# Kernel optimization log

Hardware: AMD Instinct MI355X
Metric: run time of the kernel (lower is better)

Reference implementation:

```python
import jax, jax.numpy as jnp
import numpy as np


def euler_xyz_to_matrix(angles):
    # pytorch3d euler_angles_to_matrix(angles, 'XYZ') = R_X(a0) @ R_Y(a1) @ R_Z(a2)
    ax, ay, az = angles[..., 0], angles[..., 1], angles[..., 2]
    cx, sx = jnp.cos(ax), jnp.sin(ax)
    cy, sy = jnp.cos(ay), jnp.sin(ay)
    cz, sz = jnp.cos(az), jnp.sin(az)
    one = jnp.ones_like(ax)
    zero = jnp.zeros_like(ax)
    Rx = jnp.stack([one, zero, zero, zero, cx, -sx, zero, sx, cx], axis=-1).reshape(*ax.shape, 3, 3)
    Ry = jnp.stack([cy, zero, sy, zero, one, zero, -sy, zero, cy], axis=-1).reshape(*ax.shape, 3, 3)
    Rz = jnp.stack([cz, -sz, zero, sz, cz, zero, zero, zero, one], axis=-1).reshape(*ax.shape, 3, 3)
    return Rx @ Ry @ Rz


def chamfer_bidir(x, y):
    # x, y: [R, I, N, 3]. Squared-distance chamfer, mean point reduction, per (R,I) batch.
    x2 = jnp.sum(x * x, axis=-1)  # [R,I,N]
    y2 = jnp.sum(y * y, axis=-1)  # [R,I,N]
    # d2[r,i,n,m] = |x_n - y_m|^2
    d2 = x2[..., :, None] + y2[..., None, :] - 2.0 * jnp.einsum('rind,rimd->rinm', x, y)
    cham_x = jnp.mean(jnp.min(d2, axis=-1), axis=-1)  # x -> nearest y
    cham_y = jnp.mean(jnp.min(d2, axis=-2), axis=-1)  # y -> nearest x
    return cham_x + cham_y  # [R, I]


def setup_inputs() -> dict:
    key = jax.random.key(0)
    k1, k2, k3, k4 = jax.random.split(key, 4)
    R, I, N = 4, 16, 2048
    source_points = jax.random.normal(k1, (R, I, N, 3), dtype=jnp.float32)
    target_points = jax.random.normal(k2, (I, N, 3), dtype=jnp.float32)
    rotation = 0.1 * jax.random.normal(k3, (R, I, 3), dtype=jnp.float32)
    translation = 0.1 * jax.random.normal(k4, (R, I, 3), dtype=jnp.float32)
    scale = jnp.ones((R, I), dtype=jnp.float32)
    return {
        'source_points': source_points,
        'target_points': target_points,
        'rotation': rotation,
        'translation': translation,
        'scale': scale,
    }


def reference(source_points, target_points, rotation, translation, scale):
    R, I, N, _ = source_points.shape
    rot = euler_xyz_to_matrix(rotation)  # [R,I,3,3]
    # Transform per original: 4x4 matrix with rows [:3,:] scaled by `scale`,
    # so p' = scale * (rot @ p + translation).
    transformed = scale[..., None, None] * (
        jnp.einsum('rind,rikd->rink', source_points, rot) + translation[..., None, :]
    )  # [R,I,N,3]
    # target_points [I,N,3] broadcast to [R,I,N,3] (original repeats along R)
    target = jnp.broadcast_to(target_points[None], transformed.shape)
    # original calls chamfer_distance(target, transformed): x=target, y=transformed
    return chamfer_bidir(target, transformed)  # [R, I]
```

## Files before the change

kernel.cpp:

```cpp
#include <hip/hip_runtime.h>
#include <math.h>

#define RDIM 4
#define IDIM 16
#define NPAIR 64
#define NPTS 2048
#define THREADS 256
#define ROWSB 256
#define RBLK (NPTS / ROWSB)
#define TILES (NPTS / 32)
#define SCRS 68
#define ONEBF 0x3F80u

typedef __attribute__((ext_vector_type(8))) short bf16x8;
typedef __attribute__((ext_vector_type(16))) float f32x16;
typedef __attribute__((ext_vector_type(4))) float f32x4;


__device__ __forceinline__ unsigned int f2bf(float f) {
    union { float f; unsigned int u; } v; v.f = f;
    return (v.u + 0x7FFFu + ((v.u >> 16) & 1u)) >> 16;
}
__device__ __forceinline__ float bf2f(unsigned int h) {
    union { unsigned int u; float f; } v; v.u = h << 16; return v.f;
}

__device__ __forceinline__ void make_rot(const float* __restrict__ rotv, int pair,
                                         float& r00, float& r01, float& r02,
                                         float& r10, float& r11, float& r12,
                                         float& r20, float& r21, float& r22) {
    const float ax = rotv[pair * 3 + 0];
    const float ay = rotv[pair * 3 + 1];
    const float az = rotv[pair * 3 + 2];
    float sx, cx, sy, cy, sz, cz;
    sincosf(ax, &sx, &cx);
    sincosf(ay, &sy, &cy);
    sincosf(az, &sz, &cz);
    r00 = cy * cz;                r01 = -cy * sz;               r02 = sy;
    r10 = cx * sz + sx * sy * cz; r11 = cx * cz - sx * sy * sz; r12 = -sx * cy;
    r20 = sx * sz - cx * sy * cz; r21 = sx * cz + cx * sy * sz; r22 = cx * cy;
}

__device__ __forceinline__ uint4 brec(float v0, float v1, float v2) {
    const float b0 = -2.0f * v0, b1 = -2.0f * v1, b2 = -2.0f * v2;
    const unsigned int h0 = f2bf(b0), h1 = f2bf(b1), h2 = f2bf(b2);
    const unsigned int l0 = f2bf(b0 - bf2f(h0));
    const unsigned int l1 = f2bf(b1 - bf2f(h1));
    const unsigned int l2 = f2bf(b2 - bf2f(h2));
    const float n2 = v0 * v0 + v1 * v1 + v2 * v2;
    const unsigned int nh = f2bf(n2), nl = f2bf(n2 - bf2f(nh));
    return make_uint4(h0 | (h1 << 16), h2 | (l0 << 16), l1 | (l2 << 16), nh | (nl << 16));
}

__global__ __launch_bounds__(THREADS)
void prep(const float* __restrict__ src, const float* __restrict__ tgt,
          const float* __restrict__ rotv, const float* __restrict__ trav,
          const float* __restrict__ scal,
          uint4* __restrict__ Yb, uint4* __restrict__ Xb)
{
    const int b = blockIdx.x;
    const int tid = threadIdx.x;
    if (b < NPAIR) {
        const int pair = b;
        float r00, r01, r02, r10, r11, r12, r20, r21, r22;
        make_rot(rotv, pair, r00, r01, r02, r10, r11, r12, r20, r21, r22);
        const float t0 = trav[pair * 3 + 0];
        const float t1 = trav[pair * 3 + 1];
        const float t2 = trav[pair * 3 + 2];
        const float s  = scal[pair];
        const float* __restrict__ srcp = src + (size_t)pair * NPTS * 3;
#pragma unroll
        for (int u = 0; u < NPTS / THREADS; ++u) {
            const int m = u * THREADS + tid;
            const float p0 = srcp[m * 3 + 0];
            const float p1 = srcp[m * 3 + 1];
            const float p2 = srcp[m * 3 + 2];
            const float y0 = s * fmaf(r00, p0, fmaf(r01, p1, fmaf(r02, p2, t0)));
            const float y1 = s * fmaf(r10, p0, fmaf(r11, p1, fmaf(r12, p2, t1)));
            const float y2 = s * fmaf(r20, p0, fmaf(r21, p1, fmaf(r22, p2, t2)));
            Yb[(size_t)pair * NPTS + m] = brec(y0, y1, y2);
        }
    } else {
        const int i = b - NPAIR;
        const float* __restrict__ tgtp = tgt + (size_t)i * NPTS * 3;
#pragma unroll
        for (int u = 0; u < NPTS / THREADS; ++u) {
            const int m = u * THREADS + tid;
            Xb[(size_t)i * NPTS + m] = brec(tgtp[m * 3 + 0], tgtp[m * 3 + 1], tgtp[m * 3 + 2]);
        }
    }
}

__global__ __launch_bounds__(THREADS, 3)
void chamfer_main(const float* __restrict__ src, const float* __restrict__ tgt,
                  const float* __restrict__ rotv, const float* __restrict__ trav,
                  const float* __restrict__ scal,
                  const uint4* __restrict__ Yb, const uint4* __restrict__ Xb,
                  float* __restrict__ out)
{
    __shared__ alignas(16) unsigned char smem[34816 + 8192];
    __shared__ float rowq2[ROWSB];
    __shared__ float wsum[4];
    unsigned short* sB = (unsigned short*)smem;
    float* scratch = (float*)smem;
    unsigned short* sA = (unsigned short*)(smem + 34816);

    const int pair  = blockIdx.x;
    const int rb    = blockIdx.y;
    const int passB = blockIdx.z;
    const int i     = pair & (IDIM - 1);
    const int tid   = threadIdx.x;
    const int lane  = tid & 63;
    const int w     = tid >> 6;
    const int c31   = lane & 31;
    const int h     = lane >> 5;

    const uint4* __restrict__ gB = (passB == 0) ? (Yb + (size_t)pair * NPTS)
                                                : (Xb + (size_t)i * NPTS);
#pragma unroll
    for (int j = 0; j < 8; ++j)
        ((uint4*)sB)[j * THREADS + tid] = gB[j * THREADS + tid];

    {
        const int n = rb * ROWSB + tid;
        float q0, q1, q2v;
        if (passB == 0) {
            const float* __restrict__ tgtp = tgt + (size_t)i * NPTS * 3;
            q0 = tgtp[n * 3 + 0]; q1 = tgtp[n * 3 + 1]; q2v = tgtp[n * 3 + 2];
        } else {
            float r00, r01, r02, r10, r11, r12, r20, r21, r22;
            make_rot(rotv, pair, r00, r01, r02, r10, r11, r12, r20, r21, r22);
            const float t0 = trav[pair * 3 + 0];
            const float t1 = trav[pair * 3 + 1];
            const float t2 = trav[pair * 3 + 2];
            const float s  = scal[pair];
            const float* __restrict__ srcp = src + (size_t)pair * NPTS * 3;
            const float p0 = srcp[n * 3 + 0];
            const float p1 = srcp[n * 3 + 1];
            const float p2 = srcp[n * 3 + 2];
            q0  = s * fmaf(r00, p0, fmaf(r01, p1, fmaf(r02, p2, t0)));
            q1  = s * fmaf(r10, p0, fmaf(r11, p1, fmaf(r12, p2, t1)));
            q2v = s * fmaf(r20, p0, fmaf(r21, p1, fmaf(r22, p2, t2)));
        }
        rowq2[tid] = q0 * q0 + q1 * q1 + q2v * q2v;
        const unsigned int h0 = f2bf(q0), h1 = f2bf(q1), h2 = f2bf(q2v);
        const unsigned int l0 = f2bf(q0 - bf2f(h0));
        const unsigned int l1 = f2bf(q1 - bf2f(h1));
        const unsigned int l2 = f2bf(q2v - bf2f(h2));
        uint4* rk = (uint4*)&sA[tid * 16];
        rk[0] = make_uint4(h0 | (h1 << 16), h2 | (l0 << 16), l1 | (l2 << 16), ONEBF);
        rk[1] = make_uint4(l0 | (l1 << 16), l2 | (h0 << 16), h1 | (h2 << 16), ONEBF << 16);
    }
    __syncthreads();

    bf16x8 af0 = *(const bf16x8*)&sA[(w * 64 + c31) * 16 + h * 8];
    bf16x8 af1 = *(const bf16x8*)&sA[(w * 64 + 32 + c31) * 16 + h * 8];

    float mn0[16], mn1[16];
#pragma unroll
    for (int j = 0; j < 16; ++j) { mn0[j] = 3.4e38f; mn1[j] = 3.4e38f; }

    const f32x16 zero16 = {0,0,0,0, 0,0,0,0, 0,0,0,0, 0,0,0,0};

#pragma unroll 2
    for (int t2 = 0; t2 < TILES / 2; ++t2) {
        const bf16x8 bfA = *(const bf16x8*)&sB[((t2 * 2 + 0) * 32 + c31) * 8];
        const bf16x8 bfB = *(const bf16x8*)&sB[((t2 * 2 + 1) * 32 + c31) * 8];
        const f32x16 d0a = __builtin_amdgcn_mfma_f32_32x32x16_bf16(af0, bfA, zero16, 0, 0, 0);
        const f32x16 d0b = __builtin_amdgcn_mfma_f32_32x32x16_bf16(af0, bfB, zero16, 0, 0, 0);
#pragma unroll
        for (int j = 0; j < 16; ++j)
            mn0[j] = fminf(mn0[j], fminf(d0a[j], d0b[j]));
        const f32x16 d1a = __builtin_amdgcn_mfma_f32_32x32x16_bf16(af1, bfA, zero16, 0, 0, 0);
        const f32x16 d1b = __builtin_amdgcn_mfma_f32_32x32x16_bf16(af1, bfB, zero16, 0, 0, 0);
#pragma unroll
        for (int j = 0; j < 16; ++j)
            mn1[j] = fminf(mn1[j], fminf(d1a[j], d1b[j]));
    }
    __syncthreads();

#pragma unroll
    for (int g2 = 0; g2 < 4; ++g2) {
        f32x4 v4;
        v4[0] = mn0[g2 * 4 + 0]; v4[1] = mn0[g2 * 4 + 1];
        v4[2] = mn0[g2 * 4 + 2]; v4[3] = mn0[g2 * 4 + 3];
        *(f32x4*)&scratch[(w * 32 + c31) * SCRS + 8 * g2 + 4 * h] = v4;
        v4[0] = mn1[g2 * 4 + 0]; v4[1] = mn1[g2 * 4 + 1];
        v4[2] = mn1[g2 * 4 + 2]; v4[3] = mn1[g2 * 4 + 3];
        *(f32x4*)&scratch[(w * 32 + c31) * SCRS + 32 + 8 * g2 + 4 * h] = v4;
    }
    __syncthreads();

    float m = scratch[(w * 32) * SCRS + lane];
#pragma unroll
    for (int c = 1; c < 32; ++c)
        m = fminf(m, scratch[(w * 32 + c) * SCRS + lane]);
    float v = m + rowq2[tid];

#pragma unroll
    for (int off = 32; off > 0; off >>= 1)
        v += __shfl_down(v, off, 64);
    if (lane == 0) wsum[w] = v;
    __syncthreads();
    if (tid == 0) {
        const float tot = wsum[0] + wsum[1] + wsum[2] + wsum[3];
        atomicAdd(&out[pair], tot * (1.0f / NPTS));
    }
}

extern "C" void kernel_launch(void* const* d_in, const int* in_sizes, int n_in,
                              void* d_out, int out_size, void* d_ws, size_t ws_size,
                              hipStream_t stream) {
    const float* src  = (const float*)d_in[0];
    const float* tgt  = (const float*)d_in[1];
    const float* rotv = (const float*)d_in[2];
    const float* trav = (const float*)d_in[3];
    const float* scal = (const float*)d_in[4];
    float* out = (float*)d_out;

    char* ws = (char*)d_ws;
    uint4* Yb = (uint4*)ws;
    uint4* Xb = (uint4*)(ws + (size_t)NPAIR * NPTS * 16);

    hipMemsetAsync(out, 0, NPAIR * sizeof(float), stream);

    prep<<<NPAIR + IDIM, THREADS, 0, stream>>>(src, tgt, rotv, trav, scal, Yb, Xb);

    dim3 grid(NPAIR, RBLK, 2);
    chamfer_main<<<grid, THREADS, 0, stream>>>(src, tgt, rotv, trav, scal, Yb, Xb, out);
}
```

Before: 98.77 us.

## Shrink LDS footprint to fit four blocks per CU and build A fragments in registers

Each lane now builds its own MFMA A-operand fragment in registers by recomputing the transformed point, so the shared-memory A staging area goes away. The reduction scratch uses an XOR-free rotated layout that fits inside the 32KB B buffer, and the per-row squared norms stay in registers. The end-of-block reduction is replaced by one atomicAdd per wave. Together these cut LDS use enough to raise the launch-bounds occupancy hint from 3 to 4 blocks per CU, at the cost of redundant point loads and transforms plus four times as many atomics.

```diff
diff --git a/kernel.cpp b/kernel.cpp
--- a/kernel.cpp
+++ b/kernel.cpp
@@ -9,13 +9,10 @@
 #define ROWSB 256
 #define RBLK (NPTS / ROWSB)
 #define TILES (NPTS / 32)
-#define SCRS 68
 #define ONEBF 0x3F80u
 
 typedef __attribute__((ext_vector_type(8))) short bf16x8;
 typedef __attribute__((ext_vector_type(16))) float f32x16;
-typedef __attribute__((ext_vector_type(4))) float f32x4;
-
 
 __device__ __forceinline__ unsigned int f2bf(float f) {
     union { float f; unsigned int u; } v; v.f = f;
@@ -91,19 +88,16 @@
     }
 }
 
-__global__ __launch_bounds__(THREADS, 3)
+__global__ __launch_bounds__(THREADS, 4)
 void chamfer_main(const float* __restrict__ src, const float* __restrict__ tgt,
                   const float* __restrict__ rotv, const float* __restrict__ trav,
                   const float* __restrict__ scal,
                   const uint4* __restrict__ Yb, const uint4* __restrict__ Xb,
                   float* __restrict__ out)
 {
-    __shared__ alignas(16) unsigned char smem[34816 + 8192];
-    __shared__ float rowq2[ROWSB];
-    __shared__ float wsum[4];
+    __shared__ alignas(16) unsigned char smem[32768];
     unsigned short* sB = (unsigned short*)smem;
     float* scratch = (float*)smem;
-    unsigned short* sA = (unsigned short*)(smem + 34816);
 
     const int pair  = blockIdx.x;
     const int rb    = blockIdx.y;
@@ -121,46 +115,61 @@
     for (int j = 0; j < 8; ++j)
         ((uint4*)sB)[j * THREADS + tid] = gB[j * THREADS + tid];
 
-    {
-        const int n = rb * ROWSB + tid;
-        float q0, q1, q2v;
+    float r00, r01, r02, r10, r11, r12, r20, r21, r22, t0, t1, t2, s;
+    if (passB != 0) {
+        make_rot(rotv, pair, r00, r01, r02, r10, r11, r12, r20, r21, r22);
+        t0 = trav[pair * 3 + 0];
+        t1 = trav[pair * 3 + 1];
+        t2 = trav[pair * 3 + 2];
+        s  = scal[pair];
+    }
+    const float* __restrict__ tgtp = tgt + (size_t)i    * NPTS * 3;
+    const float* __restrict__ srcp = src + (size_t)pair * NPTS * 3;
+
+    auto getq = [&](int n, float& q0, float& q1, float& q2) {
         if (passB == 0) {
-            const float* __restrict__ tgtp = tgt + (size_t)i * NPTS * 3;
-            q0 = tgtp[n * 3 + 0]; q1 = tgtp[n * 3 + 1]; q2v = tgtp[n * 3 + 2];
+            q0 = tgtp[n * 3 + 0]; q1 = tgtp[n * 3 + 1]; q2 = tgtp[n * 3 + 2];
         } else {
-            float r00, r01, r02, r10, r11, r12, r20, r21, r22;
-            make_rot(rotv, pair, r00, r01, r02, r10, r11, r12, r20, r21, r22);
-            const float t0 = trav[pair * 3 + 0];
-            const float t1 = trav[pair * 3 + 1];
-            const float t2 = trav[pair * 3 + 2];
-            const float s  = scal[pair];
-            const float* __restrict__ srcp = src + (size_t)pair * NPTS * 3;
             const float p0 = srcp[n * 3 + 0];
             const float p1 = srcp[n * 3 + 1];
             const float p2 = srcp[n * 3 + 2];
-            q0  = s * fmaf(r00, p0, fmaf(r01, p1, fmaf(r02, p2, t0)));
-            q1  = s * fmaf(r10, p0, fmaf(r11, p1, fmaf(r12, p2, t1)));
-            q2v = s * fmaf(r20, p0, fmaf(r21, p1, fmaf(r22, p2, t2)));
+            q0 = s * fmaf(r00, p0, fmaf(r01, p1, fmaf(r02, p2, t0)));
+            q1 = s * fmaf(r10, p0, fmaf(r11, p1, fmaf(r12, p2, t1)));
+            q2 = s * fmaf(r20, p0, fmaf(r21, p1, fmaf(r22, p2, t2)));
         }
-        rowq2[tid] = q0 * q0 + q1 * q1 + q2v * q2v;
+    };
+
+    float myq2;
+    {
+        float q0, q1, q2v;
+        getq(rb * ROWSB + tid, q0, q1, q2v);
+        myq2 = q0 * q0 + q1 * q1 + q2v * q2v;
+    }
+
+    auto buildA = [&](int n) -> bf16x8 {
+        float q0, q1, q2v;
+        getq(n, q0, q1, q2v);
         const unsigned int h0 = f2bf(q0), h1 = f2bf(q1), h2 = f2bf(q2v);
         const unsigned int l0 = f2bf(q0 - bf2f(h0));
         const unsigned int l1 = f2bf(q1 - bf2f(h1));
         const unsigned int l2 = f2bf(q2v - bf2f(h2));
-        uint4* rk = (uint4*)&sA[tid * 16];
-        rk[0] = make_uint4(h0 | (h1 << 16), h2 | (l0 << 16), l1 | (l2 << 16), ONEBF);
-        rk[1] = make_uint4(l0 | (l1 << 16), l2 | (h0 << 16), h1 | (h2 << 16), ONEBF << 16);
-    }
+        union { uint4 u; bf16x8 v; } cv;
+        if (h == 0)
+            cv.u = make_uint4(h0 | (h1 << 16), h2 | (l0 << 16), l1 | (l2 << 16), ONEBF);
+        else
+            cv.u = make_uint4(l0 | (l1 << 16), l2 | (h0 << 16), h1 | (h2 << 16), ONEBF << 16);
+        return cv.v;
+    };
+    const bf16x8 af0 = buildA(rb * ROWSB + w * 64 + c31);
+    const bf16x8 af1 = buildA(rb * ROWSB + w * 64 + 32 + c31);
+
+    float mn0[16], mn1[16];
+#pragma unroll
+    for (int j = 0; j < 16; ++j) { mn0[j] = 3.4e38f; mn1[j] = 3.4e38f; }
+
+    const f32x16 zero16 = {0,0,0,0, 0,0,0,0, 0,0,0,0, 0,0,0,0};
+
     __syncthreads();
-
-    bf16x8 af0 = *(const bf16x8*)&sA[(w * 64 + c31) * 16 + h * 8];
-    bf16x8 af1 = *(const bf16x8*)&sA[(w * 64 + 32 + c31) * 16 + h * 8];
-
-    float mn0[16], mn1[16];
-#pragma unroll
-    for (int j = 0; j < 16; ++j) { mn0[j] = 3.4e38f; mn1[j] = 3.4e38f; }
-
-    const f32x16 zero16 = {0,0,0,0, 0,0,0,0, 0,0,0,0, 0,0,0,0};
 
 #pragma unroll 2
     for (int t2 = 0; t2 < TILES / 2; ++t2) {
@@ -179,33 +188,26 @@
     }
     __syncthreads();
 
-#pragma unroll
-    for (int g2 = 0; g2 < 4; ++g2) {
-        f32x4 v4;
-        v4[0] = mn0[g2 * 4 + 0]; v4[1] = mn0[g2 * 4 + 1];
-        v4[2] = mn0[g2 * 4 + 2]; v4[3] = mn0[g2 * 4 + 3];
-        *(f32x4*)&scratch[(w * 32 + c31) * SCRS + 8 * g2 + 4 * h] = v4;
-        v4[0] = mn1[g2 * 4 + 0]; v4[1] = mn1[g2 * 4 + 1];
-        v4[2] = mn1[g2 * 4 + 2]; v4[3] = mn1[g2 * 4 + 3];
-        *(f32x4*)&scratch[(w * 32 + c31) * SCRS + 32 + 8 * g2 + 4 * h] = v4;
+    float* sw = &scratch[w * 2048];
+#pragma unroll
+    for (int j = 0; j < 16; ++j) {
+        const int r0 = 8 * (j >> 2) + 4 * h + (j & 3);
+        sw[c31 * 64 + ((r0 + 5 * c31) & 63)]      = mn0[j];
+        sw[c31 * 64 + ((r0 + 32 + 5 * c31) & 63)] = mn1[j];
     }
     __syncthreads();
 
-    float m = scratch[(w * 32) * SCRS + lane];
-#pragma unroll
-    for (int c = 1; c < 32; ++c)
-        m = fminf(m, scratch[(w * 32 + c) * SCRS + lane]);
-    float v = m + rowq2[tid];
+    float m = 3.4e38f;
+#pragma unroll
+    for (int c = 0; c < 32; ++c)
+        m = fminf(m, sw[c * 64 + ((lane + 5 * c) & 63)]);
+    float v = m + myq2;
 
 #pragma unroll
     for (int off = 32; off > 0; off >>= 1)
         v += __shfl_down(v, off, 64);
-    if (lane == 0) wsum[w] = v;
-    __syncthreads();
-    if (tid == 0) {
-        const float tot = wsum[0] + wsum[1] + wsum[2] + wsum[3];
-        atomicAdd(&out[pair], tot * (1.0f / NPTS));
-    }
+    if (lane == 0)
+        atomicAdd(&out[pair], v * (1.0f / NPTS));
 }
 
 extern "C" void kernel_launch(void* const* d_in, const int* in_sizes, int n_in,
```

Result: slower. 104.2 us (+5.5%).
